# Kernel tuning notes

Measured on AMD Instinct MI355X. Metric: run time of the kernel, lower is better.

## Reference

```python
import jax, jax.numpy as jnp
import numpy as np

B, IN, OUT = 131072, 128, 32
GRID_SIZE, SPLINE_ORDER = 5, 3
GRID_LO, GRID_HI = -1.0, 1.0
N_BASIS = GRID_SIZE + SPLINE_ORDER  # 8


def _centers_and_spacing():
    n_knots = GRID_SIZE + 2 * SPLINE_ORDER + 1  # 12
    grid = jnp.linspace(GRID_LO, GRID_HI, n_knots)
    centers = grid[SPLINE_ORDER:SPLINE_ORDER + N_BASIS]  # (8,)
    spacing = (GRID_HI - GRID_LO) / GRID_SIZE + 1e-06
    return centers, spacing


def setup_inputs() -> dict:
    key = jax.random.key(0)
    k1, k2, k3 = jax.random.split(key, 3)
    x = jax.random.normal(k1, (B, IN), dtype=jnp.float32)
    coeff = jax.random.normal(k2, (IN, OUT, N_BASIS), dtype=jnp.float32) * 0.1
    base_weight = jnp.ones((IN, OUT), dtype=jnp.float32)
    base_bias = jnp.zeros((IN, OUT), dtype=jnp.float32)
    edge_weights = jax.random.normal(k3, (IN, OUT), dtype=jnp.float32) * 0.1
    return {"x": x, "coeff": coeff, "base_weight": base_weight,
            "base_bias": base_bias, "edge_weights": edge_weights}


def reference(x, coeff, base_weight, base_bias, edge_weights):
    # y[b,j] = sum_i w[i,j] * ( bw[i,j]*silu(x[b,i]) + bb[i,j]
    #                           + sum_k basis[b,i,k]*coeff[i,j,k] )
    centers, spacing = _centers_and_spacing()
    silu = x * jax.nn.sigmoid(x)                                    # (B, I)
    z = (x[:, :, None] - centers[None, None, :]) / spacing          # (B, I, K)
    basis = jnp.exp(-0.5 * z * z)                                   # (B, I, K)
    # base activation contribution
    base_out = jnp.einsum('bi,ij->bj', silu, edge_weights * base_weight)
    bias_out = jnp.sum(edge_weights * base_bias, axis=0)            # (J,)
    # spline contribution: contract over input dim i and basis dim k
    spline_out = jnp.einsum('bik,ijk->bj', basis,
                            edge_weights[:, :, None] * coeff)
    return base_out + bias_out[None, :] + spline_out
```

## Files before the change

### kernel.cpp

```cpp
#include <hip/hip_runtime.h>

typedef short bf16x8 __attribute__((ext_vector_type(8)));
typedef float f32x4v __attribute__((ext_vector_type(4)));

constexpr double H_D    = 0.4 + 1e-6;
constexpr double INVH_D = 1.0 / H_D;
constexpr double C0_D   = -1.0 + 6.0 / 11.0;
constexpr double DLT_D  = (2.0 / 11.0) / H_D;
constexpr double L2E_D  = 1.4426950408889634;

constexpr float INVH = (float)INVH_D;
constexpr float NC0H = (float)(-C0_D * INVH_D);
constexpr float A2f  = (float)(-0.5 * L2E_D);
constexpr float B2f  = (float)(DLT_D * L2E_D);
constexpr float GCF  = (float)(-0.5 * DLT_D * DLT_D * L2E_D);
constexpr float NL2E = (float)(-L2E_D);

__device__ __forceinline__ float fexp2(float v) {
#if __has_builtin(__builtin_amdgcn_exp2f)
  return __builtin_amdgcn_exp2f(v);
#else
  return exp2f(v);
#endif
}
__device__ __forceinline__ float frcp(float v) {
#if __has_builtin(__builtin_amdgcn_rcpf)
  return __builtin_amdgcn_rcpf(v);
#else
  return 1.0f / v;
#endif
}
__device__ __forceinline__ float siluf(float v) {
  return v * frcp(1.0f + fexp2(NL2E * v));
}
__device__ __forceinline__ unsigned pk2(float lo, float hi) {
  unsigned a = __float_as_uint(hi) + 0x8000u;
  unsigned b = __float_as_uint(lo) + 0x8000u;
  return __builtin_amdgcn_perm(a, b, 0x07060302u);
}
__device__ __forceinline__ bf16x8 packfrag(const float (&v)[8]) {
  uint4 d;
  d.x = pk2(v[0], v[1]);
  d.y = pk2(v[2], v[3]);
  d.z = pk2(v[4], v[5]);
  d.w = pk2(v[6], v[7]);
  return __builtin_bit_cast(bf16x8, d);
}
__device__ __forceinline__ unsigned rne16(float f) {
  unsigned u = __float_as_uint(f);
  return (u + 0x7fffu + ((u >> 16) & 1u)) >> 16;
}

__global__ void kan_prep(const float* __restrict__ coeff,
                         const float* __restrict__ bw,
                         const float* __restrict__ bb,
                         const float* __restrict__ ew,
                         uint4* __restrict__ wfrag,
                         float* __restrict__ bias) {
  if (blockIdx.x == 18) {
    __shared__ float part[256];
    const int n = threadIdx.x & 31;
    const int c = threadIdx.x >> 5;
    float s = 0.f;
#pragma unroll
    for (int i = c * 16; i < c * 16 + 16; ++i)
      s += ew[i * 32 + n] * bb[i * 32 + n];
    part[threadIdx.x] = s;
    __syncthreads();
    if (threadIdx.x < 32) {
      float t = 0.f;
#pragma unroll
      for (int c2 = 0; c2 < 8; ++c2) t += part[c2 * 32 + threadIdx.x];
      bias[threadIdx.x] = t;
    }
    return;
  }
  const int e    = blockIdx.x * 4 + (threadIdx.x >> 6);
  const int lane = threadIdx.x & 63;
  const int s = e >> 1, h = e & 1;
  const int G = s / 9, t = s % 9;
  const int n = h * 16 + (lane & 15);
  const int cbase = G * 32 + (lane >> 4) * 8;
  float v[8];
  if (t == 0) {
#pragma unroll
    for (int j = 0; j < 8; ++j) {
      int i = cbase + j;
      v[j] = ew[i * 32 + n] * bw[i * 32 + n];
    }
  } else {
    const int k = t - 1;
    const float g = exp2f(GCF * (float)(k * k));
#pragma unroll
    for (int j = 0; j < 8; ++j) {
      int i = cbase + j;
      v[j] = ew[i * 32 + n] * coeff[(i * 32 + n) * 8 + k] * g;
    }
  }
  uint4 d;
  d.x = (rne16(v[1]) << 16) | rne16(v[0]);
  d.y = (rne16(v[3]) << 16) | rne16(v[2]);
  d.z = (rne16(v[5]) << 16) | rne16(v[4]);
  d.w = (rne16(v[7]) << 16) | rne16(v[6]);
  wfrag[e * 64 + lane] = d;
}

__device__ __forceinline__ void gl_lds16(const uint4* g, uint4* l) {
  __builtin_amdgcn_global_load_lds(
      (const __attribute__((address_space(1))) void*)g,
      (__attribute__((address_space(3))) void*)l, 16, 0, 0);
}

__device__ __forceinline__ void load_x8(float (&xb)[2][8],
                                        const float* __restrict__ xbase,
                                        int coloff) {
#pragma unroll
  for (int tl = 0; tl < 2; ++tl) {
    const float4* p =
        reinterpret_cast<const float4*>(xbase + (long)tl * 16 * 128 + coloff);
    float4 a = p[0], b = p[1];
    xb[tl][0] = a.x; xb[tl][1] = a.y; xb[tl][2] = a.z; xb[tl][3] = a.w;
    xb[tl][4] = b.x; xb[tl][5] = b.y; xb[tl][6] = b.z; xb[tl][7] = b.w;
  }
}

__global__ __launch_bounds__(1024, 4) void kan_main(
    const float* __restrict__ x,
    const uint4* __restrict__ wfrag,
    const float* __restrict__ bias,
    float* __restrict__ out) {
  __shared__ uint4 wlds[4608];
  const int tid  = threadIdx.x;
  const int lane = tid & 63;
  const int wave = tid >> 6;
  const int m    = lane & 15;
  const int quad = lane >> 4;
  const long rowbase = ((long)blockIdx.x * 16 + wave) * 32;

#pragma unroll
  for (int i = 0; i < 4; ++i)
    gl_lds16(wfrag + tid + i * 1024, &wlds[tid + i * 1024]);
  if (tid < 512) gl_lds16(wfrag + 4096 + tid, &wlds[4096 + tid]);

  f32x4v acc[2][2];
#pragma unroll
  for (int tl = 0; tl < 2; ++tl)
#pragma unroll
    for (int hh = 0; hh < 2; ++hh)
#pragma unroll
      for (int rr = 0; rr < 4; ++rr) acc[tl][hh][rr] = 0.f;

  const float* xbase = x + (rowbase + m) * 128 + (long)quad * 8;

  float xb[2][8];
  load_x8(xb, xbase, 0);
  const float bv0 = bias[m];
  const float bv1 = bias[m + 16];
  __syncthreads();

#pragma unroll 1
  for (int G = 0; G < 4; ++G) {
    bf16x8 af0[2];
    float pg[2][8], rg[2][8];
#pragma unroll
    for (int tl = 0; tl < 2; ++tl) {
      float sv[8];
#pragma unroll
      for (int j = 0; j < 8; ++j) sv[j] = siluf(xb[tl][j]);
      af0[tl] = packfrag(sv);
#pragma unroll
      for (int j = 0; j < 8; ++j) {
        float u = fmaf(xb[tl][j], INVH, NC0H);
        pg[tl][j] = fexp2(A2f * u * u);
        rg[tl][j] = fexp2(B2f * u);
      }
    }

    if (G < 3) load_x8(xb, xbase, (G + 1) * 32);

    const uint4* wl = wlds + G * 1152 + lane;

#pragma unroll
    for (int tl = 0; tl < 2; ++tl) {
      acc[tl][0] = __builtin_amdgcn_mfma_f32_16x16x32_bf16(
          af0[tl], __builtin_bit_cast(bf16x8, wl[0]), acc[tl][0], 0, 0, 0);
      acc[tl][1] = __builtin_amdgcn_mfma_f32_16x16x32_bf16(
          af0[tl], __builtin_bit_cast(bf16x8, wl[64]), acc[tl][1], 0, 0, 0);
    }

#pragma unroll
    for (int t = 1; t <= 8; ++t) {
      bf16x8 c0 = __builtin_bit_cast(bf16x8, wl[t * 128]);
      bf16x8 c1 = __builtin_bit_cast(bf16x8, wl[t * 128 + 64]);
#pragma unroll
      for (int tl = 0; tl < 2; ++tl) {
        bf16x8 af = packfrag(pg[tl]);
        acc[tl][0] = __builtin_amdgcn_mfma_f32_16x16x32_bf16(af, c0, acc[tl][0], 0, 0, 0);
        acc[tl][1] = __builtin_amdgcn_mfma_f32_16x16x32_bf16(af, c1, acc[tl][1], 0, 0, 0);
        if (t < 8) {
#pragma unroll
          for (int j = 0; j < 8; ++j) pg[tl][j] *= rg[tl][j];
        }
      }
    }
  }

#pragma unroll
  for (int tl = 0; tl < 2; ++tl) {
#pragma unroll
    for (int rr = 0; rr < 4; ++rr) {
      long row = rowbase + tl * 16 + quad * 4 + rr;
      out[row * 32 + m]      = acc[tl][0][rr] + bv0;
      out[row * 32 + m + 16] = acc[tl][1][rr] + bv1;
    }
  }
}

extern "C" void kernel_launch(void* const* d_in, const int* in_sizes, int n_in,
                              void* d_out, int out_size, void* d_ws, size_t ws_size,
                              hipStream_t stream) {
  const float* x     = (const float*)d_in[0];
  const float* coeff = (const float*)d_in[1];
  const float* bw    = (const float*)d_in[2];
  const float* bb    = (const float*)d_in[3];
  const float* ew    = (const float*)d_in[4];

  uint4* wfrag = (uint4*)d_ws;
  float* bias  = (float*)((char*)d_ws + 73728);

  kan_prep<<<19, 256, 0, stream>>>(coeff, bw, bb, ew, wfrag, bias);
  kan_main<<<256, 1024, 0, stream>>>(x, wfrag, bias, (float*)d_out);
}
```

Baseline: 116.4 us.

## Prefetch all x tiles up front and halve block size to 512 threads

```diff
diff --git a/kernel.cpp b/kernel.cpp
--- a/kernel.cpp
+++ b/kernel.cpp
@@ -111,20 +111,7 @@
       (__attribute__((address_space(3))) void*)l, 16, 0, 0);
 }
 
-__device__ __forceinline__ void load_x8(float (&xb)[2][8],
-                                        const float* __restrict__ xbase,
-                                        int coloff) {
-#pragma unroll
-  for (int tl = 0; tl < 2; ++tl) {
-    const float4* p =
-        reinterpret_cast<const float4*>(xbase + (long)tl * 16 * 128 + coloff);
-    float4 a = p[0], b = p[1];
-    xb[tl][0] = a.x; xb[tl][1] = a.y; xb[tl][2] = a.z; xb[tl][3] = a.w;
-    xb[tl][4] = b.x; xb[tl][5] = b.y; xb[tl][6] = b.z; xb[tl][7] = b.w;
-  }
-}
-
-__global__ __launch_bounds__(1024, 4) void kan_main(
+__global__ __launch_bounds__(512, 2) void kan_main(
     const float* __restrict__ x,
     const uint4* __restrict__ wfrag,
     const float* __restrict__ bias,
@@ -135,48 +122,58 @@
   const int wave = tid >> 6;
   const int m    = lane & 15;
   const int quad = lane >> 4;
-  const long rowbase = ((long)blockIdx.x * 16 + wave) * 32;
-
-#pragma unroll
-  for (int i = 0; i < 4; ++i)
-    gl_lds16(wfrag + tid + i * 1024, &wlds[tid + i * 1024]);
-  if (tid < 512) gl_lds16(wfrag + 4096 + tid, &wlds[4096 + tid]);
-
-  f32x4v acc[2][2];
+  const long rowbase = ((long)blockIdx.x * 8 + wave) * 32;
+
+  const float* xbase = x + (rowbase + m) * 128 + (long)quad * 8;
+  float4 xq[2][4][2];
 #pragma unroll
   for (int tl = 0; tl < 2; ++tl)
 #pragma unroll
-    for (int hh = 0; hh < 2; ++hh)
-#pragma unroll
-      for (int rr = 0; rr < 4; ++rr) acc[tl][hh][rr] = 0.f;
-
-  const float* xbase = x + (rowbase + m) * 128 + (long)quad * 8;
-
-  float xb[2][8];
-  load_x8(xb, xbase, 0);
+    for (int G = 0; G < 4; ++G) {
+      const float4* p =
+          reinterpret_cast<const float4*>(xbase + (long)tl * 16 * 128 + G * 32);
+      xq[tl][G][0] = p[0];
+      xq[tl][G][1] = p[1];
+    }
   const float bv0 = bias[m];
   const float bv1 = bias[m + 16];
+
+#pragma unroll
+  for (int i = 0; i < 9; ++i)
+    gl_lds16(wfrag + tid + i * 512, &wlds[tid + i * 512]);
+
+  f32x4v acc[2][2];
+#pragma unroll
+  for (int tl = 0; tl < 2; ++tl)
+#pragma unroll
+    for (int hh = 0; hh < 2; ++hh)
+#pragma unroll
+      for (int rr = 0; rr < 4; ++rr) acc[tl][hh][rr] = 0.f;
+
   __syncthreads();
 
-#pragma unroll 1
+#pragma unroll
   for (int G = 0; G < 4; ++G) {
     bf16x8 af0[2];
     float pg[2][8], rg[2][8];
 #pragma unroll
     for (int tl = 0; tl < 2; ++tl) {
+      float xb[8];
+      xb[0] = xq[tl][G][0].x; xb[1] = xq[tl][G][0].y;
+      xb[2] = xq[tl][G][0].z; xb[3] = xq[tl][G][0].w;
+      xb[4] = xq[tl][G][1].x; xb[5] = xq[tl][G][1].y;
+      xb[6] = xq[tl][G][1].z; xb[7] = xq[tl][G][1].w;
       float sv[8];
 #pragma unroll
-      for (int j = 0; j < 8; ++j) sv[j] = siluf(xb[tl][j]);
+      for (int j = 0; j < 8; ++j) sv[j] = siluf(xb[j]);
       af0[tl] = packfrag(sv);
 #pragma unroll
       for (int j = 0; j < 8; ++j) {
-        float u = fmaf(xb[tl][j], INVH, NC0H);
+        float u = fmaf(xb[j], INVH, NC0H);
         pg[tl][j] = fexp2(A2f * u * u);
         rg[tl][j] = fexp2(B2f * u);
       }
     }
-
-    if (G < 3) load_x8(xb, xbase, (G + 1) * 32);
 
     const uint4* wl = wlds + G * 1152 + lane;
 
@@ -229,5 +226,5 @@
   float* bias  = (float*)((char*)d_ws + 73728);
 
   kan_prep<<<19, 256, 0, stream>>>(coeff, bw, bb, ew, wfrag, bias);
-  kan_main<<<256, 1024, 0, stream>>>(x, wfrag, bias, (float*)d_out);
-}
+  kan_main<<<512, 512, 0, stream>>>(x, wfrag, bias, (float*)d_out);
+}
```

After: 122.8 us. 1.06x slower.
